# Kernel optimization log

Hardware: AMD Instinct MI355X
Metric: run time of the kernel (lower is better)

Reference implementation:

```python
import jax, jax.numpy as jnp
import numpy as np

N, T, S, D = 50000, 8192, 16, 64
DIN = 4 * D + 3  # MLP input dim
LEAKY = 0.001


def setup_inputs() -> dict:
    key = jax.random.key(0)
    ks = jax.random.split(key, 12)
    coords = jax.random.normal(ks[0], (N, S, 3), dtype=jnp.float32)
    encoded = jax.random.normal(ks[1], (N, D), dtype=jnp.float32)
    t = jax.random.uniform(ks[2], (S,), dtype=jnp.float32)
    answer = jax.random.normal(ks[3], (N, S, 3), dtype=jnp.float32)
    # tetras: 4 distinct atom indices + chirality sign (+/-1)
    base = jax.random.randint(ks[4], (T,), 0, N - 4)
    idx4 = base[:, None] + jnp.arange(4, dtype=jnp.int32)[None, :]
    sign = 2 * jax.random.randint(ks[5], (T, 1), 0, 2) - 1
    tetras = jnp.concatenate([idx4.astype(jnp.int32), sign.astype(jnp.int32)], axis=1)
    # MLP params (Linear(DIN,D), Linear(D,D), Linear(D,D), Linear(D,2))
    def lin(k, fi, fo):
        b = 1.0 / np.sqrt(fi)
        return jax.random.uniform(k, (fi, fo), jnp.float32, -b, b)
    W1 = lin(ks[6], DIN, D); b1 = jnp.zeros((D,), jnp.float32)
    W2 = lin(ks[7], D, D);   b2 = jnp.zeros((D,), jnp.float32)
    W3 = lin(ks[8], D, D);   b3 = jnp.zeros((D,), jnp.float32)
    W4 = lin(ks[9], D, 2);   b4 = jnp.zeros((2,), jnp.float32)
    return {"coords": coords, "tetras": tetras, "encoded": encoded, "t": t,
            "answer": answer, "W1": W1, "b1": b1, "W2": W2, "b2": b2,
            "W3": W3, "b3": b3, "W4": W4, "b4": b4}


def _lrelu(x):
    return jnp.where(x >= 0, x, LEAKY * x)


def reference(coords, tetras, encoded, t, answer, W1, b1, W2, b2, W3, b3, W4, b4):
    # permutations: [3T, 5]
    perms = jnp.concatenate([tetras,
                             tetras[:, jnp.array([0, 3, 1, 2, 4])],
                             tetras[:, jnp.array([0, 2, 3, 1, 4])]], axis=0)
    idx = perms[:, :4]                      # [3T, 4]
    p = coords[idx]                         # [3T, 4, S, 3]
    v0 = p[:, 1] - p[:, 0]                  # [3T, S, 3]
    v1 = p[:, 2] - p[:, 0]
    v2 = p[:, 3] - p[:, 0]
    sign = perms[:, 4].astype(coords.dtype)[:, None, None]
    cross = sign * jnp.cross(v1, v2)        # [3T, S, 3]
    cross = cross / jnp.linalg.norm(cross, axis=-1, keepdims=True)
    sm = v1 + v2
    sm = sm / jnp.linalg.norm(sm, axis=-1, keepdims=True)
    out = jnp.sum(cross * v0, axis=-1)      # [3T, S]
    along = -jnp.sum(sm * v0, axis=-1)      # [3T, S]

    enc = encoded[idx]                      # [3T, 4, D]
    P = perms.shape[0]
    Sn = t.shape[0]
    feats = jnp.concatenate([
        jnp.broadcast_to(enc[:, 0][:, None, :], (P, Sn, D)),
        jnp.broadcast_to(enc[:, 1][:, None, :], (P, Sn, D)),
        jnp.broadcast_to(enc[:, 2][:, None, :], (P, Sn, D)),
        jnp.broadcast_to(enc[:, 3][:, None, :], (P, Sn, D)),
        jnp.broadcast_to(t[None, :, None], (P, Sn, 1)),
        out[:, :, None] / 4,
        along[:, :, None] / 4,
    ], axis=2)                              # [3T, S, 4D+3]

    h = _lrelu(feats @ W1 + b1)
    h = _lrelu(h @ W2 + b2)
    h = _lrelu(h @ W3 + b3)
    delta = h @ W4 + b4                     # [3T, S, 2]

    answer = answer.at[perms[:, 0]].add(-0.25 * delta[:, :, 0:1] * cross)
    answer = answer.at[perms[:, 1]].add(0.25 * delta[:, :, 1:2] * cross)
    return answer
```

## Files before the change

### kernel.cpp

```cpp
#include <hip/hip_runtime.h>

#define TT 8192
#define SS 16
#define DD 64
#define LEAKY 0.001f
#define PERMS (3*TT)
#define WPB 4
#define PPW 12
#define TPW 4
#define BPB (WPB*PPW)
#define NBLK (PERMS/BPB)

typedef short  short8 __attribute__((ext_vector_type(8)));
typedef __bf16 bf16x8 __attribute__((ext_vector_type(8)));
typedef float  f32x4  __attribute__((ext_vector_type(4)));

union FragU { short8 s; bf16x8 b; uint4 u; };

__device__ __forceinline__ unsigned cvtpk(float a, float b) {
  unsigned r; asm("v_cvt_pk_bf16_f32 %0, %1, %2" : "=v"(r) : "v"(a), "v"(b)); return r;
}
__device__ __forceinline__ float lrelu(float x) { return fmaxf(x, LEAKY * x); }
__device__ __forceinline__ unsigned pack_lrelu(float a, float b) {
  return cvtpk(lrelu(a), lrelu(b));
}
__device__ __forceinline__ float ulo(unsigned u) { return __builtin_bit_cast(float, u << 16); }
__device__ __forceinline__ float uhi(unsigned u) { return __builtin_bit_cast(float, u & 0xffff0000u); }
__device__ __forceinline__ float bf2f(short v) {
  return __builtin_bit_cast(float, ((unsigned)(unsigned short)v) << 16);
}
__device__ __forceinline__ short f2bf_fast(float x) {
  unsigned u = __builtin_bit_cast(unsigned, x);
  return (short)((u + 0x8000u) >> 16);
}
__device__ __forceinline__ FragU pack8c(const float* p) {
  const float4 a = *(const float4*)p;
  const float4 b = *(const float4*)(p + 4);
  FragU r;
  r.u.x = cvtpk(a.x, a.y); r.u.y = cvtpk(a.z, a.w);
  r.u.z = cvtpk(b.x, b.y); r.u.w = cvtpk(b.z, b.w);
  return r;
}
__device__ __forceinline__ FragU pack2f4(const float4 a, const float4 b) {
  FragU r;
  r.u.x = cvtpk(a.x, a.y); r.u.y = cvtpk(a.z, a.w);
  r.u.z = cvtpk(b.x, b.y); r.u.w = cvtpk(b.z, b.w);
  return r;
}

__global__ __launch_bounds__(WPB*64, 2)
void tetra_mlp_kernel(const float* __restrict__ coords,
                      const int*   __restrict__ tetras,
                      const float* __restrict__ encoded,
                      const float* __restrict__ tvec,
                      const float* __restrict__ W1, const float* __restrict__ b1,
                      const float* __restrict__ W2, const float* __restrict__ b2,
                      const float* __restrict__ W3, const float* __restrict__ b3,
                      const float* __restrict__ W4, const float* __restrict__ b4,
                      float* __restrict__ answer)
{
  __shared__ __align__(16) short w1T[64*256];
  __shared__ __align__(16) short w2f[8][64][8];
  __shared__ __align__(16) short w3f[8][64][8];
  __shared__ __align__(16) short bases[BPB*DD];
  __shared__ __align__(16) unsigned crs_[WPB][PPW*SS*2];
  __shared__ __align__(8)  unsigned oas_[WPB][PPW*SS];
  __shared__ int idxs[BPB*5];

  const int tid = threadIdx.x;

  for (int e = tid; e < 8*64; e += WPB*64) {
    const int f = e >> 6, ln = e & 63;
    const int kg2 = ln >> 4, n2 = ln & 15;
    const int ks = f >> 2, nt = f & 3;
    const int k0 = ks*32 + kg2*8;
    const int c2 = (nt & 1)*32 + (n2 >> 2)*8 + ((nt >> 1) << 2) + (n2 & 3);
    const int c3 = nt*16 + n2;
    uint4 p2, p3;
    p2.x = cvtpk(W2[(k0+0)*DD + c2], W2[(k0+1)*DD + c2]);
    p2.y = cvtpk(W2[(k0+2)*DD + c2], W2[(k0+3)*DD + c2]);
    p2.z = cvtpk(W2[(k0+4)*DD + c2], W2[(k0+5)*DD + c2]);
    p2.w = cvtpk(W2[(k0+6)*DD + c2], W2[(k0+7)*DD + c2]);
    p3.x = cvtpk(W3[(k0+0)*DD + c3], W3[(k0+1)*DD + c3]);
    p3.y = cvtpk(W3[(k0+2)*DD + c3], W3[(k0+3)*DD + c3]);
    p3.z = cvtpk(W3[(k0+4)*DD + c3], W3[(k0+5)*DD + c3]);
    p3.w = cvtpk(W3[(k0+6)*DD + c3], W3[(k0+7)*DD + c3]);
    *(uint4*)&w2f[f][ln][0] = p2;
    *(uint4*)&w3f[f][ln][0] = p3;
  }
  {
    const int n = tid & 63, arow = tid >> 6;
    #pragma unroll 4
    for (int i = 0; i < 32; ++i) {
      const int k = (i*4 + arow)*2;
      const unsigned w = cvtpk(W1[(size_t)k*DD + n], W1[(size_t)(k+1)*DD + n]);
      const int off = (n*512 + k*2) ^ ((n & 7) << 4);
      *(unsigned*)((char*)w1T + off) = w;
    }
  }
  if (tid < BPB) {
    const int wv2 = tid / PPW, lp = tid % PPW;
    const int tl = lp / 3, v = lp - tl*3;
    const int gt = blockIdx.x*(WPB*TPW) + wv2*TPW + tl;
    const int* tp = tetras + gt*5;
    const int i0 = tp[0], i1 = tp[1], i2 = tp[2], i3 = tp[3], sg = tp[4];
    int b, c, d;
    if (v == 0)      { b = i1; c = i2; d = i3; }
    else if (v == 1) { b = i3; c = i1; d = i2; }
    else             { b = i2; c = i3; d = i1; }
    int* ip = &idxs[tid*5];
    ip[0] = i0; ip[1] = b; ip[2] = c; ip[3] = d; ip[4] = sg;
  }
  __syncthreads();

  const int wv = tid >> 6, lane = tid & 63;
  const int kg = lane >> 4, n16 = lane & 15;
  unsigned* crw = crs_[wv];
  unsigned* oaw = oas_[wv];

  FragU w1t_[2], w1o_[2], w1a_[2];
  #pragma unroll
  for (int ks = 0; ks < 2; ++ks) {
    const int k = ks*32 + kg*8;
    w1t_[ks] = pack8c(W1 + 256*DD + k);
    w1o_[ks] = pack8c(W1 + 257*DD + k);
    w1a_[ks] = pack8c(W1 + 258*DD + k);
  }
  unsigned w4p[4][4];
  #pragma unroll
  for (int nt = 0; nt < 4; ++nt)
    #pragma unroll
    for (int r = 0; r < 4; ++r) {
      const int dim = nt*16 + kg*4 + r;
      w4p[nt][r] = cvtpk(W4[dim*2+0], W4[dim*2+1]);
    }
  unsigned b2p[4][2], b3p[4][2];
  #pragma unroll
  for (int nt = 0; nt < 4; ++nt)
    #pragma unroll
    for (int q = 0; q < 2; ++q) {
      const int o2 = (nt & 1)*32 + kg*8 + ((nt >> 1) << 2) + 2*q;
      const int o3 = nt*16 + kg*4 + 2*q;
      b2p[nt][q] = cvtpk(b2[o2], b2[o2+1]);
      b3p[nt][q] = cvtpk(b3[o3], b3[o3+1]);
    }
  const float b40 = b4[0], b41 = b4[1];
  const float ts_l = tvec[n16];

  {
    const int* ip = &idxs[(wv*PPW + kg*3)*5];
    const int i0 = ip[0], i1 = ip[1], i2 = ip[2], i3 = ip[3];
    const float sg = (float)ip[4];
    const int s2 = n16;
    const float* p0 = coords + ((size_t)i0*SS + s2)*3;
    const float* p1 = coords + ((size_t)i1*SS + s2)*3;
    const float* p2 = coords + ((size_t)i2*SS + s2)*3;
    const float* p3 = coords + ((size_t)i3*SS + s2)*3;
    const float a0 = p0[0], a1 = p0[1], a2 = p0[2];
    const float q10 = p1[0], q11 = p1[1], q12 = p1[2];
    const float q20 = p2[0], q21 = p2[1], q22 = p2[2];
    const float q30 = p3[0], q31 = p3[1], q32 = p3[2];
    const float e1x = q10-a0, e1y = q11-a1, e1z = q12-a2;
    const float e2x = q20-a0, e2y = q21-a1, e2z = q22-a2;
    const float e3x = q30-a0, e3y = q31-a1, e3z = q32-a2;
    #pragma unroll
    for (int v = 0; v < 3; ++v) {
      float v0x, v0y, v0z, v1x, v1y, v1z, v2x, v2y, v2z;
      if (v == 0)      { v0x=e1x;v0y=e1y;v0z=e1z; v1x=e2x;v1y=e2y;v1z=e2z; v2x=e3x;v2y=e3y;v2z=e3z; }
      else if (v == 1) { v0x=e3x;v0y=e3y;v0z=e3z; v1x=e1x;v1y=e1y;v1z=e1z; v2x=e2x;v2y=e2y;v2z=e2z; }
      else             { v0x=e2x;v0y=e2y;v0z=e2z; v1x=e3x;v1y=e3y;v1z=e3z; v2x=e1x;v2y=e1y;v2z=e1z; }
      float cx = (v1y*v2z - v1z*v2y)*sg;
      float cy = (v1z*v2x - v1x*v2z)*sg;
      float cz = (v1x*v2y - v1y*v2x)*sg;
      const float rc = rsqrtf(cx*cx + cy*cy + cz*cz);
      cx *= rc; cy *= rc; cz *= rc;
      float sx = v1x+v2x, sy = v1y+v2y, sz = v1z+v2z;
      const float rs = rsqrtf(sx*sx + sy*sy + sz*sz);
      sx *= rs; sy *= rs; sz *= rs;
      const float outv =   cx*v0x + cy*v0y + cz*v0z;
      const float alng = -(sx*v0x + sy*v0y + sz*v0z);
      const int oo = (kg*3 + v)*SS + s2;
      uint2 cr; cr.x = cvtpk(cx, cy); cr.y = cvtpk(cz, cz);
      *(uint2*)&crw[oo*2] = cr;
      oaw[oo] = cvtpk(outv*0.25f, alng*0.25f);
    }
  }

  {
    float4 encL[4][2][2];
    if (n16 < PPW) {
      const int* ip = &idxs[(wv*PPW + n16)*5];
      #pragma unroll
      for (int r = 0; r < 4; ++r) {
        const float* ep = encoded + (size_t)ip[r]*DD + kg*8;
        encL[r][0][0] = *(const float4*)(ep);
        encL[r][0][1] = *(const float4*)(ep + 4);
        encL[r][1][0] = *(const float4*)(ep + 32);
        encL[r][1][1] = *(const float4*)(ep + 36);
      }
    }
    f32x4 bD[4];
    #pragma unroll
    for (int nt = 0; nt < 4; ++nt) {
      const float bv = b1[nt*16 + n16];
      bD[nt] = (f32x4){bv, bv, bv, bv};
    }
    #pragma unroll
    for (int r = 0; r < 4; ++r) {
      #pragma unroll
      for (int ks = 0; ks < 2; ++ks) {
        FragU af;
        if (n16 < PPW) {
          af = pack2f4(encL[r][ks][0], encL[r][ks][1]);
        } else {
          af.u = (uint4){0,0,0,0};
        }
        const int k0 = r*64 + ks*32 + kg*8;
        #pragma unroll
        for (int nt = 0; nt < 4; ++nt) {
          const int n = nt*16 + n16;
          const int off = (n*512 + k0*2) ^ ((n & 7) << 4);
          FragU bfr; bfr.s = *(const short8*)((const char*)w1T + off);
          bD[nt] = __builtin_amdgcn_mfma_f32_16x16x32_bf16(af.b, bfr.b, bD[nt], 0, 0, 0);
        }
      }
    }
    #pragma unroll
    for (int nt = 0; nt < 4; ++nt)
      #pragma unroll
      for (int r = 0; r < 4; ++r) {
        const int prow = kg*4 + r;
        if (prow < PPW) bases[(wv*PPW + prow)*DD + nt*16 + n16] = f2bf_fast(bD[nt][r]);
      }
  }
  __syncthreads();

  const int s = n16;

  #pragma unroll 1
  for (int su = 0; su < TPW; ++su) {
    float c0 = 0.f, c1 = 0.f, c2 = 0.f;

    FragU a1[3][2];
    #pragma unroll
    for (int u = 0; u < 3; ++u) {
      const int pi = su*3 + u;
      const unsigned oa = oaw[pi*SS + s];
      const float o0 = ulo(oa);
      const float o1 = uhi(oa);
      #pragma unroll
      for (int ks = 0; ks < 2; ++ks) {
        const short8 bb = *(const short8*)&bases[(wv*PPW + pi)*DD + ks*32 + kg*8];
        float x[8];
        #pragma unroll
        for (int j = 0; j < 8; ++j)
          x[j] = bf2f(bb[j]) + ts_l*bf2f(w1t_[ks].s[j])
               + o0*bf2f(w1o_[ks].s[j]) + o1*bf2f(w1a_[ks].s[j]);
        a1[u][ks].u.x = pack_lrelu(x[0], x[1]);
        a1[u][ks].u.y = pack_lrelu(x[2], x[3]);
        a1[u][ks].u.z = pack_lrelu(x[4], x[5]);
        a1[u][ks].u.w = pack_lrelu(x[6], x[7]);
      }
    }

    f32x4 d2[3][4];
    #pragma unroll
    for (int u = 0; u < 3; ++u)
      #pragma unroll
      for (int nt = 0; nt < 4; ++nt)
        d2[u][nt] = (f32x4){ulo(b2p[nt][0]), uhi(b2p[nt][0]), ulo(b2p[nt][1]), uhi(b2p[nt][1])};
    #pragma unroll
    for (int ks = 0; ks < 2; ++ks)
      #pragma unroll
      for (int nt = 0; nt < 4; ++nt) {
        FragU wf; wf.s = *(const short8*)&w2f[ks*4+nt][lane][0];
        #pragma unroll
        for (int u = 0; u < 3; ++u)
          d2[u][nt] = __builtin_amdgcn_mfma_f32_16x16x32_bf16(wf.b, a1[u][ks].b, d2[u][nt], 0, 0, 0);
      }

    FragU b3f[3][2];
    #pragma unroll
    for (int u = 0; u < 3; ++u) {
      unsigned pk[4][2];
      #pragma unroll
      for (int nt = 0; nt < 4; ++nt) {
        pk[nt][0] = pack_lrelu(d2[u][nt][0], d2[u][nt][1]);
        pk[nt][1] = pack_lrelu(d2[u][nt][2], d2[u][nt][3]);
      }
      #pragma unroll
      for (int ks = 0; ks < 2; ++ks)
        b3f[u][ks].u = (uint4){pk[ks][0], pk[ks][1], pk[ks+2][0], pk[ks+2][1]};
    }

    f32x4 d3[3][4];
    #pragma unroll
    for (int u = 0; u < 3; ++u)
      #pragma unroll
      for (int nt = 0; nt < 4; ++nt)
        d3[u][nt] = (f32x4){ulo(b3p[nt][0]), uhi(b3p[nt][0]), ulo(b3p[nt][1]), uhi(b3p[nt][1])};
    #pragma unroll
    for (int ks = 0; ks < 2; ++ks)
      #pragma unroll
      for (int nt = 0; nt < 4; ++nt) {
        FragU wf; wf.s = *(const short8*)&w3f[ks*4+nt][lane][0];
        #pragma unroll
        for (int u = 0; u < 3; ++u)
          d3[u][nt] = __builtin_amdgcn_mfma_f32_16x16x32_bf16(wf.b, b3f[u][ks].b, d3[u][nt], 0, 0, 0);
      }

    #pragma unroll
    for (int u = 0; u < 3; ++u) {
      const int pi = su*3 + u;
      const int rb = (u == 0) ? 1 : ((u == 1) ? 3 : 2);
      float dd0 = 0.f, dd1 = 0.f;
      #pragma unroll
      for (int nt = 0; nt < 4; ++nt)
        #pragma unroll
        for (int r = 0; r < 4; ++r) {
          const float h = lrelu(d3[u][nt][r]);
          const unsigned w4 = w4p[nt][r];
          dd0 = fmaf(h, ulo(w4), dd0);
          dd1 = fmaf(h, uhi(w4), dd1);
        }
      dd0 += __shfl_xor(dd0, 16, 64); dd0 += __shfl_xor(dd0, 32, 64);
      dd1 += __shfl_xor(dd1, 16, 64); dd1 += __shfl_xor(dd1, 32, 64);
      const float delta0 = dd0 + b40;
      const float delta1 = dd1 + b41;

      const uint2 cr = *(const uint2*)&crw[(pi*SS + s)*2];
      const float m = (kg == 0) ? (-0.25f * delta0)
                    : ((kg == rb) ? (0.25f * delta1) : 0.f);
      c0 = fmaf(m, ulo(cr.x), c0);
      c1 = fmaf(m, uhi(cr.x), c1);
      c2 = fmaf(m, ulo(cr.y), c2);
    }

    const int i0 = idxs[(wv*PPW + su*3)*5 + 0];
    float* dst = answer + (size_t)i0*48 + lane*3;
    unsafeAtomicAdd(dst + 0, c0);
    unsafeAtomicAdd(dst + 1, c1);
    unsafeAtomicAdd(dst + 2, c2);
  }
}

extern "C" void kernel_launch(void* const* d_in, const int* in_sizes, int n_in,
                              void* d_out, int out_size, void* d_ws, size_t ws_size,
                              hipStream_t stream) {
  const float* coords  = (const float*)d_in[0];
  const int*   tetras  = (const int*)d_in[1];
  const float* encoded = (const float*)d_in[2];
  const float* tvec    = (const float*)d_in[3];
  const float* answer  = (const float*)d_in[4];
  const float* W1 = (const float*)d_in[5];
  const float* b1 = (const float*)d_in[6];
  const float* W2 = (const float*)d_in[7];
  const float* b2 = (const float*)d_in[8];
  const float* W3 = (const float*)d_in[9];
  const float* b3 = (const float*)d_in[10];
  const float* W4 = (const float*)d_in[11];
  const float* b4 = (const float*)d_in[12];
  float* out = (float*)d_out;

  hipMemcpyAsync(out, answer, sizeof(float)*(size_t)out_size,
                 hipMemcpyDeviceToDevice, stream);
  tetra_mlp_kernel<<<NBLK, WPB*64, 0, stream>>>(coords, tetras, encoded, tvec,
                                                W1, b1, W2, b2, W3, b3, W4, b4, out);
}
```

Baseline: 39.71 us.

## Halve per-block work, split W1 staging in two passes, keep geometry in registers

Halves perms per warp and tetras per warp, which doubles the block count. The W1 LDS tile shrinks to half and is staged in two phases separated by barriers. Base GEMM work is concentrated in two waves that each cover 12 perms. The cross/out/along values now stay in registers and are fetched with lane shuffles instead of per-warp LDS buffers, and the per-perm MLP loop runs one perm at a time to lower register pressure. The aim is higher occupancy and less LDS, at the cost of extra barriers, idle waves during the base GEMM, and more blocks each reloading weights.

```diff
diff --git a/kernel.cpp b/kernel.cpp
--- a/kernel.cpp
+++ b/kernel.cpp
@@ -6,8 +6,8 @@
 #define LEAKY 0.001f
 #define PERMS (3*TT)
 #define WPB 4
-#define PPW 12
-#define TPW 4
+#define PPW 6
+#define TPW 2
 #define BPB (WPB*PPW)
 #define NBLK (PERMS/BPB)
 
@@ -59,12 +59,10 @@
                       const float* __restrict__ W4, const float* __restrict__ b4,
                       float* __restrict__ answer)
 {
-  __shared__ __align__(16) short w1T[64*256];
+  __shared__ __align__(16) short w1T[64*128];
   __shared__ __align__(16) short w2f[8][64][8];
   __shared__ __align__(16) short w3f[8][64][8];
   __shared__ __align__(16) short bases[BPB*DD];
-  __shared__ __align__(16) unsigned crs_[WPB][PPW*SS*2];
-  __shared__ __align__(8)  unsigned oas_[WPB][PPW*SS];
   __shared__ int idxs[BPB*5];
 
   const int tid = threadIdx.x;
@@ -88,16 +86,6 @@
     *(uint4*)&w2f[f][ln][0] = p2;
     *(uint4*)&w3f[f][ln][0] = p3;
   }
-  {
-    const int n = tid & 63, arow = tid >> 6;
-    #pragma unroll 4
-    for (int i = 0; i < 32; ++i) {
-      const int k = (i*4 + arow)*2;
-      const unsigned w = cvtpk(W1[(size_t)k*DD + n], W1[(size_t)(k+1)*DD + n]);
-      const int off = (n*512 + k*2) ^ ((n & 7) << 4);
-      *(unsigned*)((char*)w1T + off) = w;
-    }
-  }
   if (tid < BPB) {
     const int wv2 = tid / PPW, lp = tid % PPW;
     const int tl = lp / 3, v = lp - tl*3;
@@ -111,12 +99,20 @@
     int* ip = &idxs[tid*5];
     ip[0] = i0; ip[1] = b; ip[2] = c; ip[3] = d; ip[4] = sg;
   }
+  {
+    const int n = tid & 63, arow = tid >> 6;
+    #pragma unroll 4
+    for (int i = 0; i < 16; ++i) {
+      const int kk = (i*4 + arow)*2;
+      const unsigned w = cvtpk(W1[(size_t)kk*DD + n], W1[(size_t)(kk+1)*DD + n]);
+      const int off = (n*256 + kk*2) ^ ((n & 7) << 4);
+      *(unsigned*)((char*)w1T + off) = w;
+    }
+  }
   __syncthreads();
 
   const int wv = tid >> 6, lane = tid & 63;
   const int kg = lane >> 4, n16 = lane & 15;
-  unsigned* crw = crs_[wv];
-  unsigned* oaw = oas_[wv];
 
   FragU w1t_[2], w1o_[2], w1a_[2];
   #pragma unroll
@@ -147,22 +143,20 @@
   const float b40 = b4[0], b41 = b4[1];
   const float ts_l = tvec[n16];
 
+  unsigned g0[3], g1[3], g2[3];
   {
-    const int* ip = &idxs[(wv*PPW + kg*3)*5];
+    const int tl2 = (kg < 2) ? kg : 0;
+    const int* ip = &idxs[(wv*PPW + tl2*3)*5];
     const int i0 = ip[0], i1 = ip[1], i2 = ip[2], i3 = ip[3];
     const float sg = (float)ip[4];
-    const int s2 = n16;
-    const float* p0 = coords + ((size_t)i0*SS + s2)*3;
-    const float* p1 = coords + ((size_t)i1*SS + s2)*3;
-    const float* p2 = coords + ((size_t)i2*SS + s2)*3;
-    const float* p3 = coords + ((size_t)i3*SS + s2)*3;
+    const float* p0 = coords + ((size_t)i0*SS + n16)*3;
+    const float* p1 = coords + ((size_t)i1*SS + n16)*3;
+    const float* p2 = coords + ((size_t)i2*SS + n16)*3;
+    const float* p3 = coords + ((size_t)i3*SS + n16)*3;
     const float a0 = p0[0], a1 = p0[1], a2 = p0[2];
-    const float q10 = p1[0], q11 = p1[1], q12 = p1[2];
-    const float q20 = p2[0], q21 = p2[1], q22 = p2[2];
-    const float q30 = p3[0], q31 = p3[1], q32 = p3[2];
-    const float e1x = q10-a0, e1y = q11-a1, e1z = q12-a2;
-    const float e2x = q20-a0, e2y = q21-a1, e2z = q22-a2;
-    const float e3x = q30-a0, e3y = q31-a1, e3z = q32-a2;
+    const float e1x = p1[0]-a0, e1y = p1[1]-a1, e1z = p1[2]-a2;
+    const float e2x = p2[0]-a0, e2y = p2[1]-a1, e2z = p2[2]-a2;
+    const float e3x = p3[0]-a0, e3y = p3[1]-a1, e3z = p3[2]-a2;
     #pragma unroll
     for (int v = 0; v < 3; ++v) {
       float v0x, v0y, v0z, v1x, v1y, v1z, v2x, v2y, v2z;
@@ -179,49 +173,71 @@
       sx *= rs; sy *= rs; sz *= rs;
       const float outv =   cx*v0x + cy*v0y + cz*v0z;
       const float alng = -(sx*v0x + sy*v0y + sz*v0z);
-      const int oo = (kg*3 + v)*SS + s2;
-      uint2 cr; cr.x = cvtpk(cx, cy); cr.y = cvtpk(cz, cz);
-      *(uint2*)&crw[oo*2] = cr;
-      oaw[oo] = cvtpk(outv*0.25f, alng*0.25f);
-    }
-  }
-
-  {
-    float4 encL[4][2][2];
-    if (n16 < PPW) {
-      const int* ip = &idxs[(wv*PPW + n16)*5];
-      #pragma unroll
-      for (int r = 0; r < 4; ++r) {
-        const float* ep = encoded + (size_t)ip[r]*DD + kg*8;
-        encL[r][0][0] = *(const float4*)(ep);
-        encL[r][0][1] = *(const float4*)(ep + 4);
-        encL[r][1][0] = *(const float4*)(ep + 32);
-        encL[r][1][1] = *(const float4*)(ep + 36);
-      }
-    }
-    f32x4 bD[4];
-    #pragma unroll
-    for (int nt = 0; nt < 4; ++nt) {
-      const float bv = b1[nt*16 + n16];
-      bD[nt] = (f32x4){bv, bv, bv, bv};
-    }
-    #pragma unroll
-    for (int r = 0; r < 4; ++r) {
+      g0[v] = cvtpk(cx, cy);
+      g1[v] = cvtpk(cz, cz);
+      g2[v] = cvtpk(outv*0.25f, alng*0.25f);
+    }
+  }
+
+  f32x4 bD[4];
+  #pragma unroll
+  for (int nt = 0; nt < 4; ++nt) {
+    const float bv = b1[nt*16 + n16];
+    bD[nt] = (f32x4){bv, bv, bv, bv};
+  }
+  if (wv < 2) {
+    #pragma unroll
+    for (int r = 0; r < 2; ++r) {
+      FragU afa[2];
+      if (n16 < 12) {
+        const float* ep = encoded + (size_t)idxs[(wv*12 + n16)*5 + r]*DD + kg*8;
+        afa[0] = pack2f4(*(const float4*)ep,        *(const float4*)(ep + 4));
+        afa[1] = pack2f4(*(const float4*)(ep + 32), *(const float4*)(ep + 36));
+      } else { afa[0].u = (uint4){0,0,0,0}; afa[1].u = (uint4){0,0,0,0}; }
       #pragma unroll
       for (int ks = 0; ks < 2; ++ks) {
-        FragU af;
-        if (n16 < PPW) {
-          af = pack2f4(encL[r][ks][0], encL[r][ks][1]);
-        } else {
-          af.u = (uint4){0,0,0,0};
-        }
-        const int k0 = r*64 + ks*32 + kg*8;
+        const int kk = r*64 + ks*32 + kg*8;
         #pragma unroll
         for (int nt = 0; nt < 4; ++nt) {
           const int n = nt*16 + n16;
-          const int off = (n*512 + k0*2) ^ ((n & 7) << 4);
+          const int off = (n*256 + kk*2) ^ ((n & 7) << 4);
           FragU bfr; bfr.s = *(const short8*)((const char*)w1T + off);
-          bD[nt] = __builtin_amdgcn_mfma_f32_16x16x32_bf16(af.b, bfr.b, bD[nt], 0, 0, 0);
+          bD[nt] = __builtin_amdgcn_mfma_f32_16x16x32_bf16(afa[ks].b, bfr.b, bD[nt], 0, 0, 0);
+        }
+      }
+    }
+  }
+  __syncthreads();
+  {
+    const int n = tid & 63, arow = tid >> 6;
+    #pragma unroll 4
+    for (int i = 0; i < 16; ++i) {
+      const int kk = (i*4 + arow)*2;
+      const int k = 128 + kk;
+      const unsigned w = cvtpk(W1[(size_t)k*DD + n], W1[(size_t)(k+1)*DD + n]);
+      const int off = (n*256 + kk*2) ^ ((n & 7) << 4);
+      *(unsigned*)((char*)w1T + off) = w;
+    }
+  }
+  __syncthreads();
+  if (wv < 2) {
+    #pragma unroll
+    for (int r = 2; r < 4; ++r) {
+      FragU afa[2];
+      if (n16 < 12) {
+        const float* ep = encoded + (size_t)idxs[(wv*12 + n16)*5 + r]*DD + kg*8;
+        afa[0] = pack2f4(*(const float4*)ep,        *(const float4*)(ep + 4));
+        afa[1] = pack2f4(*(const float4*)(ep + 32), *(const float4*)(ep + 36));
+      } else { afa[0].u = (uint4){0,0,0,0}; afa[1].u = (uint4){0,0,0,0}; }
+      #pragma unroll
+      for (int ks = 0; ks < 2; ++ks) {
+        const int kk = (r - 2)*64 + ks*32 + kg*8;
+        #pragma unroll
+        for (int nt = 0; nt < 4; ++nt) {
+          const int n = nt*16 + n16;
+          const int off = (n*256 + kk*2) ^ ((n & 7) << 4);
+          FragU bfr; bfr.s = *(const short8*)((const char*)w1T + off);
+          bD[nt] = __builtin_amdgcn_mfma_f32_16x16x32_bf16(afa[ks].b, bfr.b, bD[nt], 0, 0, 0);
         }
       }
     }
@@ -230,7 +246,7 @@
       #pragma unroll
       for (int r = 0; r < 4; ++r) {
         const int prow = kg*4 + r;
-        if (prow < PPW) bases[(wv*PPW + prow)*DD + nt*16 + n16] = f2bf_fast(bD[nt][r]);
+        if (prow < 12) bases[(wv*12 + prow)*DD + nt*16 + n16] = f2bf_fast(bD[nt][r]);
       }
   }
   __syncthreads();
@@ -240,14 +256,17 @@
   #pragma unroll 1
   for (int su = 0; su < TPW; ++su) {
     float c0 = 0.f, c1 = 0.f, c2 = 0.f;
-
-    FragU a1[3][2];
+    const int src = su*16 + n16;
     #pragma unroll
     for (int u = 0; u < 3; ++u) {
       const int pi = su*3 + u;
-      const unsigned oa = oaw[pi*SS + s];
+      const int rb = (u == 0) ? 1 : ((u == 1) ? 3 : 2);
+
+      const unsigned oa = __shfl(g2[u], src, 64);
       const float o0 = ulo(oa);
       const float o1 = uhi(oa);
+
+      FragU a1[2];
       #pragma unroll
       for (int ks = 0; ks < 2; ++ks) {
         const short8 bb = *(const short8*)&bases[(wv*PPW + pi)*DD + ks*32 + kg*8];
@@ -256,69 +275,52 @@
         for (int j = 0; j < 8; ++j)
           x[j] = bf2f(bb[j]) + ts_l*bf2f(w1t_[ks].s[j])
                + o0*bf2f(w1o_[ks].s[j]) + o1*bf2f(w1a_[ks].s[j]);
-        a1[u][ks].u.x = pack_lrelu(x[0], x[1]);
-        a1[u][ks].u.y = pack_lrelu(x[2], x[3]);
-        a1[u][ks].u.z = pack_lrelu(x[4], x[5]);
-        a1[u][ks].u.w = pack_lrelu(x[6], x[7]);
-      }
-    }
-
-    f32x4 d2[3][4];
-    #pragma unroll
-    for (int u = 0; u < 3; ++u)
+        a1[ks].u.x = pack_lrelu(x[0], x[1]);
+        a1[ks].u.y = pack_lrelu(x[2], x[3]);
+        a1[ks].u.z = pack_lrelu(x[4], x[5]);
+        a1[ks].u.w = pack_lrelu(x[6], x[7]);
+      }
+
+      f32x4 d2[4];
       #pragma unroll
       for (int nt = 0; nt < 4; ++nt)
-        d2[u][nt] = (f32x4){ulo(b2p[nt][0]), uhi(b2p[nt][0]), ulo(b2p[nt][1]), uhi(b2p[nt][1])};
-    #pragma unroll
-    for (int ks = 0; ks < 2; ++ks)
+        d2[nt] = (f32x4){ulo(b2p[nt][0]), uhi(b2p[nt][0]), ulo(b2p[nt][1]), uhi(b2p[nt][1])};
+      #pragma unroll
+      for (int ks = 0; ks < 2; ++ks)
+        #pragma unroll
+        for (int nt = 0; nt < 4; ++nt) {
+          FragU wf; wf.s = *(const short8*)&w2f[ks*4+nt][lane][0];
+          d2[nt] = __builtin_amdgcn_mfma_f32_16x16x32_bf16(wf.b, a1[ks].b, d2[nt], 0, 0, 0);
+        }
+      unsigned pk[4][2];
       #pragma unroll
       for (int nt = 0; nt < 4; ++nt) {
-        FragU wf; wf.s = *(const short8*)&w2f[ks*4+nt][lane][0];
-        #pragma unroll
-        for (int u = 0; u < 3; ++u)
-          d2[u][nt] = __builtin_amdgcn_mfma_f32_16x16x32_bf16(wf.b, a1[u][ks].b, d2[u][nt], 0, 0, 0);
-      }
-
-    FragU b3f[3][2];
-    #pragma unroll
-    for (int u = 0; u < 3; ++u) {
-      unsigned pk[4][2];
-      #pragma unroll
-      for (int nt = 0; nt < 4; ++nt) {
-        pk[nt][0] = pack_lrelu(d2[u][nt][0], d2[u][nt][1]);
-        pk[nt][1] = pack_lrelu(d2[u][nt][2], d2[u][nt][3]);
-      }
+        pk[nt][0] = pack_lrelu(d2[nt][0], d2[nt][1]);
+        pk[nt][1] = pack_lrelu(d2[nt][2], d2[nt][3]);
+      }
+      FragU b3f[2];
       #pragma unroll
       for (int ks = 0; ks < 2; ++ks)
-        b3f[u][ks].u = (uint4){pk[ks][0], pk[ks][1], pk[ks+2][0], pk[ks+2][1]};
-    }
-
-    f32x4 d3[3][4];
-    #pragma unroll
-    for (int u = 0; u < 3; ++u)
+        b3f[ks].u = (uint4){pk[ks][0], pk[ks][1], pk[ks+2][0], pk[ks+2][1]};
+
+      f32x4 d3[4];
       #pragma unroll
       for (int nt = 0; nt < 4; ++nt)
-        d3[u][nt] = (f32x4){ulo(b3p[nt][0]), uhi(b3p[nt][0]), ulo(b3p[nt][1]), uhi(b3p[nt][1])};
-    #pragma unroll
-    for (int ks = 0; ks < 2; ++ks)
-      #pragma unroll
-      for (int nt = 0; nt < 4; ++nt) {
-        FragU wf; wf.s = *(const short8*)&w3f[ks*4+nt][lane][0];
-        #pragma unroll
-        for (int u = 0; u < 3; ++u)
-          d3[u][nt] = __builtin_amdgcn_mfma_f32_16x16x32_bf16(wf.b, b3f[u][ks].b, d3[u][nt], 0, 0, 0);
-      }
-
-    #pragma unroll
-    for (int u = 0; u < 3; ++u) {
-      const int pi = su*3 + u;
-      const int rb = (u == 0) ? 1 : ((u == 1) ? 3 : 2);
+        d3[nt] = (f32x4){ulo(b3p[nt][0]), uhi(b3p[nt][0]), ulo(b3p[nt][1]), uhi(b3p[nt][1])};
+      #pragma unroll
+      for (int ks = 0; ks < 2; ++ks)
+        #pragma unroll
+        for (int nt = 0; nt < 4; ++nt) {
+          FragU wf; wf.s = *(const short8*)&w3f[ks*4+nt][lane][0];
+          d3[nt] = __builtin_amdgcn_mfma_f32_16x16x32_bf16(wf.b, b3f[ks].b, d3[nt], 0, 0, 0);
+        }
+
       float dd0 = 0.f, dd1 = 0.f;
       #pragma unroll
       for (int nt = 0; nt < 4; ++nt)
         #pragma unroll
         for (int r = 0; r < 4; ++r) {
-          const float h = lrelu(d3[u][nt][r]);
+          const float h = lrelu(d3[nt][r]);
           const unsigned w4 = w4p[nt][r];
           dd0 = fmaf(h, ulo(w4), dd0);
           dd1 = fmaf(h, uhi(w4), dd1);
@@ -328,12 +330,13 @@
       const float delta0 = dd0 + b40;
       const float delta1 = dd1 + b41;
 
-      const uint2 cr = *(const uint2*)&crw[(pi*SS + s)*2];
+      const unsigned cra = __shfl(g0[u], src, 64);
+      const unsigned crb = __shfl(g1[u], src, 64);
       const float m = (kg == 0) ? (-0.25f * delta0)
                     : ((kg == rb) ? (0.25f * delta1) : 0.f);
-      c0 = fmaf(m, ulo(cr.x), c0);
-      c1 = fmaf(m, uhi(cr.x), c1);
-      c2 = fmaf(m, ulo(cr.y), c2);
+      c0 = fmaf(m, ulo(cra), c0);
+      c1 = fmaf(m, uhi(cra), c1);
+      c2 = fmaf(m, ulo(crb), c2);
     }
 
     const int i0 = idxs[(wv*PPW + su*3)*5 + 0];
```

Measured after the change: 51.22 us. 29.0% more time.
